# Kernel optimization log

Hardware: AMD Instinct MI355X
Metric: run time of the kernel (lower is better)

## Reference

```python
import jax, jax.numpy as jnp
import numpy as np

K = 7      # kernel_size
PAD = 3    # padding ('same' with stride 1)
G = 16     # groups


def _unfold(x):
    """torch nn.Unfold equivalent, stride=1, dilation=1.
    Returns [B, C, K*K, H, W] with kernel positions ordered (kh, kw),
    matching torch's (c, kh, kw) channel-major layout after reshape."""
    B, C, H, W = x.shape
    xp = jnp.pad(x, ((0, 0), (0, 0), (PAD, PAD), (PAD, PAD)))
    patches = jnp.stack(
        [xp[:, :, i:i + H, j:j + W] for i in range(K) for j in range(K)],
        axis=2,
    )
    return patches


def setup_inputs() -> dict:
    key = jax.random.key(0)
    k1, k2, k3 = jax.random.split(key, 3)
    B, C, H, W = 4, 256, 64, 64
    x = jax.random.normal(k1, (B, C, H, W), dtype=jnp.float32)
    # 1x1 conv producing kernel_prod*groups = 49*16 = 784 channels (with bias)
    w_kernel = jax.random.normal(k2, (G * K * K, C), dtype=jnp.float32) * 0.05
    b_kernel = jax.random.normal(k3, (G * K * K,), dtype=jnp.float32) * 0.05
    return {"x": x, "w_kernel": w_kernel, "b_kernel": b_kernel}


def reference(x, w_kernel, b_kernel):
    B, C, H, W = x.shape
    Cg = C // G
    # unfolded input: [B, G, C//G, K*K, H, W]
    patches = _unfold(x).reshape(B, G, Cg, K * K, H, W)
    # dynamic per-pixel kernel: AvgPool(k=1) is identity at stride 1,
    # then 1x1 conv with bias -> [B, G*K*K, H, W]
    kern = jnp.einsum('bchw,kc->bkhw', x, w_kernel) + b_kernel[None, :, None, None]
    kern = kern.reshape(B, G, 1, K * K, H, W)
    # multiply and sum-reduce over kernel positions, flatten groups
    out = (patches * kern).sum(axis=3).reshape(B, C, H, W)
    return out
```

## Files before the change

### kernel.cpp

```cpp
#include <hip/hip_runtime.h>


#define B_   4
#define C_   256
#define G_   16
#define KK_  49
#define KS_  7
#define PD_  3

#define XP8_BYTES (B_*32*4096*8*2)
#define WBF_OFF   XP8_BYTES

#define SKW   28
#define HC_   70
#define HPOS  (10*HC_)

typedef __attribute__((ext_vector_type(8))) short bf16x8;
typedef __attribute__((ext_vector_type(4))) float f32x4;
typedef unsigned short ushort_t;

__device__ inline unsigned f2bf(float f) {
    unsigned u = __float_as_uint(f);
    u += 0x7FFF + ((u >> 16) & 1);
    return u >> 16;
}

__global__ __launch_bounds__(256)
void cvt_xp8(const float* __restrict__ x, const float* __restrict__ wk,
             ushort_t* __restrict__ xp8, unsigned* __restrict__ wbf) {
    const int t = threadIdx.x;
    if (blockIdx.x == 64) {
        const int slice = blockIdx.z * 4 + blockIdx.y;
        const float2* wk2 = (const float2*)wk;
        const int base = slice * 6272;
        for (int k = t; k < 6272; k += 256) {
            float2 v = wk2[base + k];
            wbf[base + k] = f2bf(v.x) | (f2bf(v.y) << 16);
        }
        return;
    }
    __shared__ float tile[64][65];
    const int p0 = blockIdx.x * 64;
    const int c0 = blockIdx.y * 64;
    const int b  = blockIdx.z;
    const int px_r = t & 63;
    #pragma unroll
    for (int i = 0; i < 16; ++i) {
        int ch = (t >> 6) + i * 4;
        tile[ch][px_r] = x[((size_t)(b * C_ + c0 + ch) << 12) + p0 + px_r];
    }
    __syncthreads();
    const int px = t & 63;
    const int ob = t >> 6;
    #pragma unroll
    for (int jj = 0; jj < 2; ++jj) {
        const int j = ob + jj * 4;
        unsigned u[4];
        #pragma unroll
        for (int k2 = 0; k2 < 4; ++k2) {
            float a0 = tile[j * 8 + 2 * k2][px];
            float a1 = tile[j * 8 + 2 * k2 + 1][px];
            u[k2] = f2bf(a0) | (f2bf(a1) << 16);
        }
        ushort_t* dst = xp8 + (((size_t)((b << 5) + (c0 >> 3) + j) << 12) + p0 + px) * 8;
        *(uint4*)dst = make_uint4(u[0], u[1], u[2], u[3]);
    }
}

__device__ inline uint4 stage_ld(const ushort_t* __restrict__ xp8,
                                 int b, int oct, int gy0, int e) {
    const int row = e / HC_;
    const int col = e - row * HC_;
    const int sy = gy0 + row - PD_;
    const int sx = col - PD_;
    if (sy >= 0 && sy < 64 && sx >= 0 && sx < 64)
        return *(const uint4*)(xp8 + (((size_t)((b << 5) + oct) << 12) + sy * 64 + sx) * 8);
    return make_uint4(0u, 0u, 0u, 0u);
}

__global__ __launch_bounds__(256, 4)
void inv_fused(const ushort_t* __restrict__ xp8,
               const ushort_t* __restrict__ wbf,
               const float* __restrict__ bk,
               float* __restrict__ out) {
    __shared__ unsigned kern2[256 * SKW];
    __shared__ unsigned halo4[HPOS * 4];

    const int bid  = blockIdx.x;
    const int g    = bid >> 6;
    const int b    = (bid >> 4) & 3;
    const int tile = bid & 15;
    const int gy0  = tile * 4;
    const int p0   = tile * 256;

    const int tid  = threadIdx.x;
    const int wv   = tid >> 6;
    const int ln15 = tid & 15;
    const int quad = (tid & 63) >> 4;

    f32x4 acc[16];
    #pragma unroll
    for (int i = 0; i < 16; ++i) acc[i] = (f32x4){0.f, 0.f, 0.f, 0.f};

    const ushort_t* ap[4];
    #pragma unroll
    for (int mt = 0; mt < 4; ++mt) {
        int r = mt * 16 + ln15; if (r > KK_ - 1) r = KK_ - 1;
        ap[mt] = wbf + (size_t)(g * KK_ + r) * C_ + quad * 8;
    }
    const ushort_t* bp = xp8 + (((size_t)((b << 5) + quad) << 12) + p0 + wv * 64 + ln15) * 8;

    bf16x8 af[3][4], bf[3][4];
    #pragma unroll
    for (int kb = 0; kb < 2; ++kb) {
        const int cc = kb * 32;
        #pragma unroll
        for (int mt = 0; mt < 4; ++mt)
            af[kb][mt] = *(const bf16x8*)(ap[mt] + cc);
        #pragma unroll
        for (int nt = 0; nt < 4; ++nt)
            bf[kb][nt] = *(const bf16x8*)(bp + ((size_t)cc << 12) + nt * 128);
    }

    #pragma unroll
    for (int k = 0; k < 8; ++k) {
        const int cur = k % 3;
        if (k < 6) {
            const int nxt = (k + 2) % 3;
            const int cc  = (k + 2) * 32;
            #pragma unroll
            for (int mt = 0; mt < 4; ++mt)
                af[nxt][mt] = *(const bf16x8*)(ap[mt] + cc);
            #pragma unroll
            for (int nt = 0; nt < 4; ++nt)
                bf[nxt][nt] = *(const bf16x8*)(bp + ((size_t)cc << 12) + nt * 128);
        }
        #pragma unroll
        for (int mt = 0; mt < 4; ++mt) {
            #pragma unroll
            for (int nt = 0; nt < 4; ++nt) {
                acc[mt * 4 + nt] = __builtin_amdgcn_mfma_f32_16x16x32_bf16(
                    af[cur][mt], bf[cur][nt], acc[mt * 4 + nt], 0, 0, 0);
            }
        }
    }

    for (int e = tid; e < HPOS; e += 256)
        *(uint4*)&halo4[e * 4] = stage_ld(xp8, b, 2 * g, gy0, e);

    #pragma unroll
    for (int mt = 0; mt < 3; ++mt) {
        const int m0 = mt * 16 + quad * 4;
        const float b0 = bk[g * KK_ + m0],     b1 = bk[g * KK_ + m0 + 1];
        const float b2 = bk[g * KK_ + m0 + 2], b3 = bk[g * KK_ + m0 + 3];
        #pragma unroll
        for (int nt = 0; nt < 4; ++nt) {
            const int p = wv * 64 + nt * 16 + ln15;
            uint2 d;
            d.x = f2bf(acc[mt * 4 + nt][0] + b0) | (f2bf(acc[mt * 4 + nt][1] + b1) << 16);
            d.y = f2bf(acc[mt * 4 + nt][2] + b2) | (f2bf(acc[mt * 4 + nt][3] + b3) << 16);
            *(uint2*)&kern2[p * SKW + mt * 8 + quad * 2] = d;
        }
    }
    if (quad == 0) {
        const float b48 = bk[g * KK_ + 48];
        #pragma unroll
        for (int nt = 0; nt < 4; ++nt) {
            const int p = wv * 64 + nt * 16 + ln15;
            kern2[p * SKW + 24] = f2bf(acc[12 + nt][0] + b48);
        }
    }
    __syncthreads();

    float kv[KK_];
    {
        const uint4* kr = (const uint4*)&kern2[tid * SKW];
        unsigned kd[28];
        #pragma unroll
        for (int q = 0; q < 7; ++q) {
            uint4 h = kr[q];
            kd[4*q] = h.x; kd[4*q+1] = h.y; kd[4*q+2] = h.z; kd[4*q+3] = h.w;
        }
        #pragma unroll
        for (int k = 0; k < KK_; ++k) {
            unsigned d = kd[k >> 1];
            kv[k] = __uint_as_float((k & 1) ? (d & 0xffff0000u) : (d << 16));
        }
    }

    uint4 pf0 = stage_ld(xp8, b, 2 * g + 1, gy0, tid);
    uint4 pf1 = stage_ld(xp8, b, 2 * g + 1, gy0, tid + 256);
    uint4 pf2 = (tid < HPOS - 512) ? stage_ld(xp8, b, 2 * g + 1, gy0, tid + 512)
                                   : make_uint4(0u, 0u, 0u, 0u);

    const int py = tid >> 6, px = tid & 63;

    #pragma unroll 1
    for (int hb = 0; hb < 2; ++hb) {
        if (hb) {
            __syncthreads();
            *(uint4*)&halo4[tid * 4] = pf0;
            *(uint4*)&halo4[(tid + 256) * 4] = pf1;
            if (tid < HPOS - 512) *(uint4*)&halo4[(tid + 512) * 4] = pf2;
            __syncthreads();
        }
        float a[8];
        #pragma unroll
        for (int q = 0; q < 8; ++q) a[q] = 0.f;
        #pragma unroll
        for (int kh = 0; kh < KS_; ++kh) {
            const uint4* hr = (const uint4*)&halo4[((py + kh) * HC_ + px) * 4];
            #pragma unroll
            for (int kw = 0; kw < KS_; ++kw) {
                uint4 hv = hr[kw];
                float kk = kv[kh * KS_ + kw];
                a[0] = fmaf(__uint_as_float(hv.x << 16), kk, a[0]);
                a[1] = fmaf(__uint_as_float(hv.x),       kk, a[1]);
                a[2] = fmaf(__uint_as_float(hv.y << 16), kk, a[2]);
                a[3] = fmaf(__uint_as_float(hv.y),       kk, a[3]);
                a[4] = fmaf(__uint_as_float(hv.z << 16), kk, a[4]);
                a[5] = fmaf(__uint_as_float(hv.z),       kk, a[5]);
                a[6] = fmaf(__uint_as_float(hv.w << 16), kk, a[6]);
                a[7] = fmaf(__uint_as_float(hv.w),       kk, a[7]);
            }
        }
        const size_t o = ((size_t)(b * C_ + g * 16 + hb * 8) << 12) + p0 + tid;
        #pragma unroll
        for (int q = 0; q < 8; ++q)
            out[o + ((size_t)q << 12)] = a[q];
    }
}

extern "C" void kernel_launch(void* const* d_in, const int* in_sizes, int n_in,
                              void* d_out, int out_size, void* d_ws, size_t ws_size,
                              hipStream_t stream) {
    const float* x  = (const float*)d_in[0];
    const float* wk = (const float*)d_in[1];
    const float* bk = (const float*)d_in[2];
    float* o = (float*)d_out;

    ushort_t* xp8 = (ushort_t*)d_ws;
    unsigned* wbf = (unsigned*)((char*)d_ws + WBF_OFF);

    cvt_xp8<<<dim3(65, 4, B_), dim3(256), 0, stream>>>(x, wk, xp8, wbf);
    inv_fused<<<dim3(1024), dim3(256), 0, stream>>>(
        xp8, (const ushort_t*)wbf, bk, o);
}
```

Before: 104.5 us.

## Double block size to 512 threads and process both channel halves concurrently

The fused kernel now launches 512 threads per block. The GEMM work is split so each wave handles 32 pixels instead of 64, which halves the per-thread accumulators and B fragments. Both 8-channel halo halves are staged into a doubled shared buffer at once, and each 256-thread half computes one channel octet, replacing the sequential two-pass loop and its extra barriers. This exposes more parallelism and cuts per-thread register pressure, at the cost of doubled halo LDS and larger blocks that may reduce the number of resident blocks.

Measured after the change: 111.1 us. 6.4% more time.

```diff
diff --git a/kernel.cpp b/kernel.cpp
--- a/kernel.cpp
+++ b/kernel.cpp
@@ -78,13 +78,13 @@
     return make_uint4(0u, 0u, 0u, 0u);
 }
 
-__global__ __launch_bounds__(256, 4)
+__global__ __launch_bounds__(512, 4)
 void inv_fused(const ushort_t* __restrict__ xp8,
                const ushort_t* __restrict__ wbf,
                const float* __restrict__ bk,
                float* __restrict__ out) {
     __shared__ unsigned kern2[256 * SKW];
-    __shared__ unsigned halo4[HPOS * 4];
+    __shared__ unsigned halo4[2 * HPOS * 4];
 
     const int bid  = blockIdx.x;
     const int g    = bid >> 6;
@@ -98,9 +98,9 @@
     const int ln15 = tid & 15;
     const int quad = (tid & 63) >> 4;
 
-    f32x4 acc[16];
-    #pragma unroll
-    for (int i = 0; i < 16; ++i) acc[i] = (f32x4){0.f, 0.f, 0.f, 0.f};
+    f32x4 acc[8];
+    #pragma unroll
+    for (int i = 0; i < 8; ++i) acc[i] = (f32x4){0.f, 0.f, 0.f, 0.f};
 
     const ushort_t* ap[4];
     #pragma unroll
@@ -108,45 +108,52 @@
         int r = mt * 16 + ln15; if (r > KK_ - 1) r = KK_ - 1;
         ap[mt] = wbf + (size_t)(g * KK_ + r) * C_ + quad * 8;
     }
-    const ushort_t* bp = xp8 + (((size_t)((b << 5) + quad) << 12) + p0 + wv * 64 + ln15) * 8;
-
-    bf16x8 af[3][4], bf[3][4];
+    const ushort_t* bp = xp8 + (((size_t)((b << 5) + quad) << 12) + p0 + wv * 32 + ln15) * 8;
+
+    bf16x8 af[2][4], bf[3][2];
+    #pragma unroll
+    for (int mt = 0; mt < 4; ++mt)
+        af[0][mt] = *(const bf16x8*)(ap[mt]);
     #pragma unroll
     for (int kb = 0; kb < 2; ++kb) {
-        const int cc = kb * 32;
-        #pragma unroll
-        for (int mt = 0; mt < 4; ++mt)
-            af[kb][mt] = *(const bf16x8*)(ap[mt] + cc);
-        #pragma unroll
-        for (int nt = 0; nt < 4; ++nt)
-            bf[kb][nt] = *(const bf16x8*)(bp + ((size_t)cc << 12) + nt * 128);
+        #pragma unroll
+        for (int nt = 0; nt < 2; ++nt)
+            bf[kb][nt] = *(const bf16x8*)(bp + ((size_t)(kb * 32) << 12) + nt * 128);
     }
 
     #pragma unroll
     for (int k = 0; k < 8; ++k) {
-        const int cur = k % 3;
-        if (k < 6) {
-            const int nxt = (k + 2) % 3;
-            const int cc  = (k + 2) * 32;
+        const int ca = k & 1;
+        const int cb = k % 3;
+        if (k < 7) {
+            const int cc = (k + 1) * 32;
             #pragma unroll
             for (int mt = 0; mt < 4; ++mt)
-                af[nxt][mt] = *(const bf16x8*)(ap[mt] + cc);
+                af[ca ^ 1][mt] = *(const bf16x8*)(ap[mt] + cc);
+        }
+        if (k < 6) {
+            const int cc = (k + 2) * 32;
             #pragma unroll
-            for (int nt = 0; nt < 4; ++nt)
-                bf[nxt][nt] = *(const bf16x8*)(bp + ((size_t)cc << 12) + nt * 128);
+            for (int nt = 0; nt < 2; ++nt)
+                bf[(k + 2) % 3][nt] = *(const bf16x8*)(bp + ((size_t)cc << 12) + nt * 128);
         }
         #pragma unroll
         for (int mt = 0; mt < 4; ++mt) {
             #pragma unroll
-            for (int nt = 0; nt < 4; ++nt) {
-                acc[mt * 4 + nt] = __builtin_amdgcn_mfma_f32_16x16x32_bf16(
-                    af[cur][mt], bf[cur][nt], acc[mt * 4 + nt], 0, 0, 0);
+            for (int nt = 0; nt < 2; ++nt) {
+                acc[mt * 2 + nt] = __builtin_amdgcn_mfma_f32_16x16x32_bf16(
+                    af[ca][mt], bf[cb][nt], acc[mt * 2 + nt], 0, 0, 0);
             }
         }
     }
 
-    for (int e = tid; e < HPOS; e += 256)
-        *(uint4*)&halo4[e * 4] = stage_ld(xp8, b, 2 * g, gy0, e);
+    uint4 h0 = stage_ld(xp8, b, 2 * g, gy0, tid);
+    const int e1 = tid + 512;
+    uint4 h1 = (e1 < HPOS) ? stage_ld(xp8, b, 2 * g, gy0, e1)
+                           : stage_ld(xp8, b, 2 * g + 1, gy0, e1 - HPOS);
+    const int e2 = tid + 1024;
+    uint4 h2 = (e2 < 2 * HPOS) ? stage_ld(xp8, b, 2 * g + 1, gy0, e2 - HPOS)
+                               : make_uint4(0u, 0u, 0u, 0u);
 
     #pragma unroll
     for (int mt = 0; mt < 3; ++mt) {
@@ -154,27 +161,33 @@
         const float b0 = bk[g * KK_ + m0],     b1 = bk[g * KK_ + m0 + 1];
         const float b2 = bk[g * KK_ + m0 + 2], b3 = bk[g * KK_ + m0 + 3];
         #pragma unroll
-        for (int nt = 0; nt < 4; ++nt) {
-            const int p = wv * 64 + nt * 16 + ln15;
+        for (int nt = 0; nt < 2; ++nt) {
+            const int p = wv * 32 + nt * 16 + ln15;
             uint2 d;
-            d.x = f2bf(acc[mt * 4 + nt][0] + b0) | (f2bf(acc[mt * 4 + nt][1] + b1) << 16);
-            d.y = f2bf(acc[mt * 4 + nt][2] + b2) | (f2bf(acc[mt * 4 + nt][3] + b3) << 16);
+            d.x = f2bf(acc[mt * 2 + nt][0] + b0) | (f2bf(acc[mt * 2 + nt][1] + b1) << 16);
+            d.y = f2bf(acc[mt * 2 + nt][2] + b2) | (f2bf(acc[mt * 2 + nt][3] + b3) << 16);
             *(uint2*)&kern2[p * SKW + mt * 8 + quad * 2] = d;
         }
     }
     if (quad == 0) {
         const float b48 = bk[g * KK_ + 48];
         #pragma unroll
-        for (int nt = 0; nt < 4; ++nt) {
-            const int p = wv * 64 + nt * 16 + ln15;
-            kern2[p * SKW + 24] = f2bf(acc[12 + nt][0] + b48);
-        }
-    }
+        for (int nt = 0; nt < 2; ++nt) {
+            const int p = wv * 32 + nt * 16 + ln15;
+            kern2[p * SKW + 24] = f2bf(acc[6 + nt][0] + b48);
+        }
+    }
+
+    *(uint4*)&halo4[tid * 4] = h0;
+    *(uint4*)&halo4[(tid + 512) * 4] = h1;
+    if (tid < 2 * HPOS - 1024) *(uint4*)&halo4[(tid + 1024) * 4] = h2;
+
     __syncthreads();
 
+    const int pix = tid & 255;
     float kv[KK_];
     {
-        const uint4* kr = (const uint4*)&kern2[tid * SKW];
+        const uint4* kr = (const uint4*)&kern2[pix * SKW];
         unsigned kd[28];
         #pragma unroll
         for (int q = 0; q < 7; ++q) {
@@ -188,47 +201,33 @@
         }
     }
 
-    uint4 pf0 = stage_ld(xp8, b, 2 * g + 1, gy0, tid);
-    uint4 pf1 = stage_ld(xp8, b, 2 * g + 1, gy0, tid + 256);
-    uint4 pf2 = (tid < HPOS - 512) ? stage_ld(xp8, b, 2 * g + 1, gy0, tid + 512)
-                                   : make_uint4(0u, 0u, 0u, 0u);
-
-    const int py = tid >> 6, px = tid & 63;
-
-    #pragma unroll 1
-    for (int hb = 0; hb < 2; ++hb) {
-        if (hb) {
-            __syncthreads();
-            *(uint4*)&halo4[tid * 4] = pf0;
-            *(uint4*)&halo4[(tid + 256) * 4] = pf1;
-            if (tid < HPOS - 512) *(uint4*)&halo4[(tid + 512) * 4] = pf2;
-            __syncthreads();
-        }
-        float a[8];
-        #pragma unroll
-        for (int q = 0; q < 8; ++q) a[q] = 0.f;
-        #pragma unroll
-        for (int kh = 0; kh < KS_; ++kh) {
-            const uint4* hr = (const uint4*)&halo4[((py + kh) * HC_ + px) * 4];
-            #pragma unroll
-            for (int kw = 0; kw < KS_; ++kw) {
-                uint4 hv = hr[kw];
-                float kk = kv[kh * KS_ + kw];
-                a[0] = fmaf(__uint_as_float(hv.x << 16), kk, a[0]);
-                a[1] = fmaf(__uint_as_float(hv.x),       kk, a[1]);
-                a[2] = fmaf(__uint_as_float(hv.y << 16), kk, a[2]);
-                a[3] = fmaf(__uint_as_float(hv.y),       kk, a[3]);
-                a[4] = fmaf(__uint_as_float(hv.z << 16), kk, a[4]);
-                a[5] = fmaf(__uint_as_float(hv.z),       kk, a[5]);
-                a[6] = fmaf(__uint_as_float(hv.w << 16), kk, a[6]);
-                a[7] = fmaf(__uint_as_float(hv.w),       kk, a[7]);
-            }
-        }
-        const size_t o = ((size_t)(b * C_ + g * 16 + hb * 8) << 12) + p0 + tid;
-        #pragma unroll
-        for (int q = 0; q < 8; ++q)
-            out[o + ((size_t)q << 12)] = a[q];
-    }
+    const int ho = tid >> 8;
+    const int py = pix >> 6, px = pix & 63;
+
+    float a[8];
+    #pragma unroll
+    for (int q = 0; q < 8; ++q) a[q] = 0.f;
+    #pragma unroll
+    for (int kh = 0; kh < KS_; ++kh) {
+        const uint4* hr = (const uint4*)&halo4[(ho * HPOS + (py + kh) * HC_ + px) * 4];
+        #pragma unroll
+        for (int kw = 0; kw < KS_; ++kw) {
+            uint4 hv = hr[kw];
+            float kk = kv[kh * KS_ + kw];
+            a[0] = fmaf(__uint_as_float(hv.x << 16), kk, a[0]);
+            a[1] = fmaf(__uint_as_float(hv.x),       kk, a[1]);
+            a[2] = fmaf(__uint_as_float(hv.y << 16), kk, a[2]);
+            a[3] = fmaf(__uint_as_float(hv.y),       kk, a[3]);
+            a[4] = fmaf(__uint_as_float(hv.z << 16), kk, a[4]);
+            a[5] = fmaf(__uint_as_float(hv.z),       kk, a[5]);
+            a[6] = fmaf(__uint_as_float(hv.w << 16), kk, a[6]);
+            a[7] = fmaf(__uint_as_float(hv.w),       kk, a[7]);
+        }
+    }
+    const size_t o = ((size_t)(b * C_ + g * 16 + ho * 8) << 12) + p0 + pix;
+    #pragma unroll
+    for (int q = 0; q < 8; ++q)
+        out[o + ((size_t)q << 12)] = a[q];
 }
 
 extern "C" void kernel_launch(void* const* d_in, const int* in_sizes, int n_in,
@@ -243,6 +242,6 @@
     unsigned* wbf = (unsigned*)((char*)d_ws + WBF_OFF);
 
     cvt_xp8<<<dim3(65, 4, B_), dim3(256), 0, stream>>>(x, wk, xp8, wbf);
-    inv_fused<<<dim3(1024), dim3(256), 0, stream>>>(
+    inv_fused<<<dim3(1024), dim3(512), 0, stream>>>(
         xp8, (const ushort_t*)wbf, bk, o);
 }
```
